# Performance work log

Measured on AMD Instinct MI355X. Metric: run time of the kernel, lower is better.

## Reference

```python
import jax, jax.numpy as jnp
import numpy as np

EPS = 1e-5

def _ln(x, g, b):
    m = jnp.mean(x, axis=-1, keepdims=True)
    v = jnp.var(x, axis=-1, keepdims=True)
    return (x - m) / jnp.sqrt(v + EPS) * g + b

def _lin(x, w, b):
    # torch-style weight [out, in]
    return x @ w.T + b

def _mlp(x, w1, b1, w2, b2):
    # Mlp: Linear -> exact GELU -> Linear (dropout=0)
    return _lin(jax.nn.gelu(_lin(x, w1, b1), approximate=False), w2, b2)

def setup_inputs() -> dict:
    B, C, H, W = 2, 256, 64, 64
    key = jax.random.key(0)
    ks = jax.random.split(key, 32)
    s = 0.02  # param init scale keeps attention logits in a sane range
    d = {
        'center_fea': jax.random.normal(ks[0], (B, C, H, W), jnp.float32),
        'wh_fea':     jax.random.normal(ks[1], (B, C, H, W), jnp.float32),
        'cls_fea':    jax.random.normal(ks[2], (B, C, H, W), jnp.float32),
        'mix_w': jax.random.normal(ks[3], (C, 3 * C), jnp.float32) * s,
        'mix_b': jnp.zeros((C,), jnp.float32),
        'ln_g': jnp.ones((C,), jnp.float32),
        'ln_b': jnp.zeros((C,), jnp.float32),
        'q1_w': jax.random.normal(ks[4], (C, C), jnp.float32) * s,
        'q1_b': jnp.zeros((C,), jnp.float32),
        'q2_w': jax.random.normal(ks[5], (C, C), jnp.float32) * s,
        'q2_b': jnp.zeros((C,), jnp.float32),
        'q3_w': jax.random.normal(ks[6], (C, C), jnp.float32) * s,
        'q3_b': jnp.zeros((C,), jnp.float32),
        'k_w': jax.random.normal(ks[7], (C, C), jnp.float32) * s,
        'k_b': jnp.zeros((C,), jnp.float32),
        'v_w': jax.random.normal(ks[8], (C, C), jnp.float32) * s,
        'v_b': jnp.zeros((C,), jnp.float32),
        'cmlp_w1': jax.random.normal(ks[9], (C, C), jnp.float32) * s,
        'cmlp_b1': jnp.zeros((C,), jnp.float32),
        'cmlp_w2': jax.random.normal(ks[10], (C, C), jnp.float32) * s,
        'cmlp_b2': jnp.zeros((C,), jnp.float32),
        'wmlp_w1': jax.random.normal(ks[11], (C, C), jnp.float32) * s,
        'wmlp_b1': jnp.zeros((C,), jnp.float32),
        'wmlp_w2': jax.random.normal(ks[12], (C, C), jnp.float32) * s,
        'wmlp_b2': jnp.zeros((C,), jnp.float32),
        'clsmlp_w1': jax.random.normal(ks[13], (C, C), jnp.float32) * s,
        'clsmlp_b1': jnp.zeros((C,), jnp.float32),
        'clsmlp_w2': jax.random.normal(ks[14], (C, C), jnp.float32) * s,
        'clsmlp_b2': jnp.zeros((C,), jnp.float32),
    }
    return d

def reference(center_fea, wh_fea, cls_fea, mix_w, mix_b, ln_g, ln_b,
              q1_w, q1_b, q2_w, q2_b, q3_w, q3_b, k_w, k_b, v_w, v_b,
              cmlp_w1, cmlp_b1, cmlp_w2, cmlp_b2,
              wmlp_w1, wmlp_b1, wmlp_w2, wmlp_b2,
              clsmlp_w1, clsmlp_b1, clsmlp_w2, clsmlp_b2):
    b, c, h, w = center_fea.shape
    # 1x1 conv mix over concatenated channels [b, 3c, h, w] -> [b, c, h, w]
    cat = jnp.concatenate([center_fea, wh_fea, cls_fea], axis=1)
    mix = jnp.einsum('oc,bchw->bohw', mix_w, cat) + mix_b[None, :, None, None]

    tok = lambda x: x.reshape(b, c, h * w).transpose(0, 2, 1)  # [b, N, c]
    cf, wf, clf, mf = tok(center_fea), tok(wh_fea), tok(cls_fea), tok(mix)

    ct, wt, clt, mt = _ln(cf, ln_g, ln_b), _ln(wf, ln_g, ln_b), _ln(clf, ln_g, ln_b), _ln(mf, ln_g, ln_b)

    kf = _lin(mt, k_w, k_b)  # shared K
    vf = _lin(mt, v_w, v_b)  # shared V

    def attend(q):
        score = jax.nn.softmax(jnp.einsum('bnd,bmd->bnm', q, kf), axis=-1)  # [b, N, N]
        return jnp.einsum('bnm,bmd->bnd', score, vf)

    cf  = _ln(cf  + attend(_lin(ct,  q1_w, q1_b)), ln_g, ln_b)
    wf  = _ln(wf  + attend(_lin(wt,  q2_w, q2_b)), ln_g, ln_b)
    clf = _ln(clf + attend(_lin(clt, q3_w, q3_b)), ln_g, ln_b)

    cf  = _ln(cf  + _mlp(cf,  cmlp_w1, cmlp_b1, cmlp_w2, cmlp_b2), ln_g, ln_b)
    wf  = _ln(wf  + _mlp(wf,  wmlp_w1, wmlp_b1, wmlp_w2, wmlp_b2), ln_g, ln_b)
    clf = _ln(clf + _mlp(clf, clsmlp_w1, clsmlp_b1, clsmlp_w2, clsmlp_b2), ln_g, ln_b)

    untok = lambda x: x.transpose(0, 2, 1).reshape(b, c, h, w)
    return (untok(cf), untok(wf), untok(clf))
```

## Files before the change

### kernel.cpp

```cpp
#include <hip/hip_runtime.h>
#include <hip/hip_bf16.h>
#include <math.h>

typedef unsigned int   u32;
typedef unsigned short u16;
typedef float floatx4 __attribute__((ext_vector_type(4)));
typedef short bf16x8  __attribute__((ext_vector_type(8)));

#define MFMA16(a,b,c) __builtin_amdgcn_mfma_f32_16x16x32_bf16((a),(b),(c),0,0,0)

static __device__ __forceinline__ float bfbits2f(u16 h){
    return __uint_as_float(((u32)h) << 16);
}
static __device__ __forceinline__ u16 f2bfbits(float f){
    u32 u = __float_as_uint(f);
    u32 r = (u + 0x7fffu + ((u >> 16) & 1u)) >> 16;
    return (u16)r;
}
static __device__ __forceinline__ bool sniff_bf16(const void* ln_g){
    return ((const u32*)ln_g)[0] == 0x3f803f80u;
}

typedef __attribute__((address_space(1))) const unsigned int gas_u32;
typedef __attribute__((address_space(3))) unsigned int las_u32;
static __device__ __forceinline__ void gl_lds16(const void* g, void* l){
    __builtin_amdgcn_global_load_lds((gas_u32*)g, (las_u32*)l, 16, 0, 0);
}

#define DPPF(v, ctrl) __uint_as_float((u32)__builtin_amdgcn_update_dpp( \
        (int)__float_as_uint(v), (int)__float_as_uint(v), (ctrl), 0xf, 0xf, true))

static __device__ __forceinline__ float red16_max(float v){
    v = fmaxf(v, DPPF(v, 0xB1));
    v = fmaxf(v, DPPF(v, 0x4E));
    v = fmaxf(v, DPPF(v, 0x141));
    v = fmaxf(v, DPPF(v, 0x140));
    return v;
}
static __device__ __forceinline__ float red16_sum(float v){
    v += DPPF(v, 0xB1);
    v += DPPF(v, 0x4E);
    v += DPPF(v, 0x141);
    v += DPPF(v, 0x140);
    return v;
}

struct PackJob { const void* src; void* dst; int n; int mode; };
struct PackParams { PackJob jobs[26]; const void* lng; };

__global__ __launch_bounds__(256) void k_pack(PackParams p){
    bool isb = sniff_bf16(p.lng);
    PackJob j = p.jobs[blockIdx.y];
    for (int i = blockIdx.x * 256 + threadIdx.x; i < j.n; i += 256 * 256){
        float v = isb ? bfbits2f(((const u16*)j.src)[i]) : ((const float*)j.src)[i];
        if (j.mode == 0) ((u16*)j.dst)[i]  = f2bfbits(v);
        else             ((float*)j.dst)[i] = v;
    }
}

struct FtParams { const void* src[3]; u16* dst[3]; const void* lng; };

__global__ __launch_bounds__(256) void k_feat_t(FtParams p){
    bool isb = sniff_bf16(p.lng);
    int z = blockIdx.z; int si = z >> 1; int b = z & 1;
    const void* src = p.src[si]; u16* dst = p.dst[si];
    int n0 = blockIdx.x * 64, c0 = blockIdx.y * 64;
    __shared__ float tile[64][65];
    int t = threadIdx.x; int tx = t & 63; int ty = t >> 6;
    #pragma unroll
    for (int pp = 0; pp < 16; ++pp){
        int cl = ty + pp * 4;
        size_t off = ((size_t)b * 256 + c0 + cl) * 4096 + n0 + tx;
        float v = isb ? bfbits2f(((const u16*)src)[off]) : ((const float*)src)[off];
        tile[cl][tx] = v;
    }
    __syncthreads();
    #pragma unroll
    for (int pp = 0; pp < 16; ++pp){
        int nl = ty + pp * 4; int cl = tx;
        dst[((size_t)b * 4096 + n0 + nl) * 256 + c0 + cl] = f2bfbits(tile[cl][nl]);
    }
}

struct GemmJob { const u16* A0; const u16* A1; const u16* A2;
                 const u16* W; const float* bias; const u16* res; u16* out; };
struct GemmParams { GemmJob jobs[5]; int K; int op; };

__global__ __launch_bounds__(256, 4) void k_gemm(GemmParams p){
    GemmJob j = p.jobs[blockIdx.z];
    int m0 = blockIdx.x * 64, n0 = blockIdx.y * 64;
    __shared__ __align__(16) u16 As[2][64][64];
    __shared__ __align__(16) u16 Bs[2][64][64];
    int t = threadIdx.x;
    int wave = t >> 6, lane = t & 63, l15 = lane & 15, quad = lane >> 4;
    int mh = (wave & 1) * 32, nh = (wave >> 1) * 32;
    int key = l15 & 7;

    auto stage = [&](int bi, int k0){
        const u16* Ap = (k0 < 256) ? j.A0 : (k0 < 512 ? j.A1 : j.A2);
        int koff = k0 & 255;
        #pragma unroll
        for (int i = 0; i < 2; ++i){
            int rq = wave * 2 + i;
            int r  = rq * 8 + (lane >> 3);
            int gs = (lane & 7) ^ (r & 7);
            gl_lds16(Ap  + (size_t)(m0 + r) * 256 + koff + gs * 8, &As[bi][rq * 8][0]);
            gl_lds16(j.W + (size_t)(n0 + r) * p.K + k0   + gs * 8, &Bs[bi][rq * 8][0]);
        }
    };

    floatx4 acc[2][2];
    #pragma unroll
    for (int a = 0; a < 2; ++a)
        #pragma unroll
        for (int bq = 0; bq < 2; ++bq) acc[a][bq] = (floatx4){0.f,0.f,0.f,0.f};

    stage(0, 0);
    __syncthreads();
    int nk = p.K >> 6, buf = 0;

    for (int ks = 0; ks < nk; ++ks){
        if (ks + 1 < nk) stage(buf ^ 1, (ks + 1) * 64);
        #pragma unroll
        for (int kc = 0; kc < 2; ++kc){
            int gsel = ((kc * 4 + quad) ^ key) * 8;
            bf16x8 a0 = *(const bf16x8*)&As[buf][mh +      l15][gsel];
            bf16x8 a1 = *(const bf16x8*)&As[buf][mh + 16 + l15][gsel];
            bf16x8 b0 = *(const bf16x8*)&Bs[buf][nh +      l15][gsel];
            bf16x8 b1 = *(const bf16x8*)&Bs[buf][nh + 16 + l15][gsel];
            acc[0][0] = MFMA16(a0, b0, acc[0][0]);
            acc[0][1] = MFMA16(a0, b1, acc[0][1]);
            acc[1][0] = MFMA16(a1, b0, acc[1][0]);
            acc[1][1] = MFMA16(a1, b1, acc[1][1]);
        }
        __syncthreads();
        buf ^= 1;
    }

    #pragma unroll
    for (int mb = 0; mb < 2; ++mb)
        #pragma unroll
        for (int nb = 0; nb < 2; ++nb){
            int col = n0 + nh + nb * 16 + l15;
            float bias = j.bias[col];
            #pragma unroll
            for (int rg = 0; rg < 4; ++rg){
                int row = m0 + mh + mb * 16 + quad * 4 + rg;
                float v = acc[mb][nb][rg] + bias;
                if (p.op == 1)      v = 0.5f * v * (1.0f + erff(v * 0.70710678118f));
                else if (p.op == 2) v += bfbits2f(j.res[(size_t)row * 256 + col]);
                j.out[(size_t)row * 256 + col] = f2bfbits(v);
            }
        }
}

struct LnJob { const u16* src; u16* dst; };
struct LnParams { LnJob jobs[4]; const float* g; const float* b; };

__global__ __launch_bounds__(256, 4) void k_ln(LnParams p){
    LnJob j = p.jobs[blockIdx.y];
    int g16 = threadIdx.x >> 4, l = threadIdx.x & 15;
    size_t tok = (size_t)blockIdx.x * 16 + g16;
    const u16* row = j.src + tok * 256 + l * 16;
    uint4 ra = *(const uint4*)(row);
    uint4 rb = *(const uint4*)(row + 8);
    u32 wv[8] = {ra.x, ra.y, ra.z, ra.w, rb.x, rb.y, rb.z, rb.w};
    float va[16];
    float s1 = 0.f, s2 = 0.f;
    #pragma unroll
    for (int i = 0; i < 8; ++i){
        float a = bfbits2f((u16)(wv[i] & 0xffffu));
        float c = bfbits2f((u16)(wv[i] >> 16));
        va[2*i] = a; va[2*i+1] = c;
        s1 += a + c; s2 += a*a + c*c;
    }
    s1 = red16_sum(s1); s2 = red16_sum(s2);
    float mean = s1 * (1.f/256.f);
    float var  = s2 * (1.f/256.f) - mean * mean;
    float rstd = rsqrtf(var + 1e-5f);
    int c0 = l * 16;
    u32 ow[8];
    #pragma unroll
    for (int i = 0; i < 8; ++i){
        float x0 = (va[2*i]   - mean) * rstd * p.g[c0 + 2*i]     + p.b[c0 + 2*i];
        float x1 = (va[2*i+1] - mean) * rstd * p.g[c0 + 2*i + 1] + p.b[c0 + 2*i + 1];
        ow[i] = (u32)f2bfbits(x0) | ((u32)f2bfbits(x1) << 16);
    }
    u16* dst = j.dst + tok * 256 + c0;
    *(uint4*)(dst)     = (uint4){ow[0], ow[1], ow[2], ow[3]};
    *(uint4*)(dst + 8) = (uint4){ow[4], ow[5], ow[6], ow[7]};
}

struct LnOutParams { const u16* Z[3]; void* out; const float* g; const float* b; const void* lng; };

__global__ __launch_bounds__(256, 4) void k_ln_out(LnOutParams p){
    bool isb = sniff_bf16(p.lng);
    int y = blockIdx.y; int s = y >> 1, b = y & 1;
    const u16* Z = p.Z[s] + (size_t)b * 4096 * 256;
    int tok0 = blockIdx.x * 64;
    __shared__ u16 tile[64][258];
    int t = threadIdx.x, g16 = t >> 4, l = t & 15;
    #pragma unroll
    for (int pass = 0; pass < 4; ++pass){
        int tl = pass * 16 + g16;
        const u16* row = Z + (size_t)(tok0 + tl) * 256 + l * 16;
        uint4 ra = *(const uint4*)(row);
        uint4 rb = *(const uint4*)(row + 8);
        u32 wv[8] = {ra.x, ra.y, ra.z, ra.w, rb.x, rb.y, rb.z, rb.w};
        float va[16];
        float s1 = 0.f, s2 = 0.f;
        #pragma unroll
        for (int i = 0; i < 8; ++i){
            float a = bfbits2f((u16)(wv[i] & 0xffffu));
            float c = bfbits2f((u16)(wv[i] >> 16));
            va[2*i] = a; va[2*i+1] = c;
            s1 += a + c; s2 += a*a + c*c;
        }
        s1 = red16_sum(s1); s2 = red16_sum(s2);
        float mean = s1 * (1.f/256.f);
        float var  = s2 * (1.f/256.f) - mean * mean;
        float rstd = rsqrtf(var + 1e-5f);
        int c0 = l * 16;
        u32* drow = (u32*)&tile[tl][c0];
        #pragma unroll
        for (int i = 0; i < 8; ++i){
            float x0 = (va[2*i]   - mean) * rstd * p.g[c0 + 2*i]     + p.b[c0 + 2*i];
            float x1 = (va[2*i+1] - mean) * rstd * p.g[c0 + 2*i + 1] + p.b[c0 + 2*i + 1];
            drow[i] = (u32)f2bfbits(x0) | ((u32)f2bfbits(x1) << 16);
        }
    }
    __syncthreads();
    size_t obase = ((size_t)s * 2 + b) * 256 * 4096;
    int cq = t >> 6, tl2 = t & 63;
    #pragma unroll
    for (int pp = 0; pp < 64; ++pp){
        int c = pp * 4 + cq;
        u16 raw = tile[tl2][c];
        size_t off = obase + (size_t)c * 4096 + tok0 + tl2;
        if (isb) ((u16*)p.out)[off]   = raw;
        else     ((float*)p.out)[off] = bfbits2f(raw);
    }
}

__global__ __launch_bounds__(256, 4) void k_vt(const u16* __restrict__ Vf, u16* __restrict__ Vt){
    int b = blockIdx.z;
    int n0 = blockIdx.x * 64, c0 = blockIdx.y * 64;
    __shared__ u16 tile[64][66];
    int t = threadIdx.x; int tx = t & 63; int ty = t >> 6;
    #pragma unroll
    for (int pp = 0; pp < 16; ++pp){
        int nl = ty + pp * 4;
        tile[nl][tx] = Vf[((size_t)b * 4096 + n0 + nl) * 256 + c0 + tx];
    }
    __syncthreads();
    #pragma unroll
    for (int pp = 0; pp < 16; ++pp){
        int cl = ty + pp * 4; int nl = tx;
        Vt[((size_t)b * 256 + c0 + cl) * 4096 + n0 + nl] = tile[nl][cl];
    }
}

struct FlashParams {
    const u16* Q[3]; const u16* K; const u16* Vt;
    const u16* Res[3]; u16* Out[3];
    const float* g; const float* b;
};

__global__ __launch_bounds__(256, 2) void k_flash(FlashParams p){
    int s = blockIdx.y >> 1, b = blockIdx.y & 1;
    int m0 = blockIdx.x * 64;
    const u16* Q   = p.Q[s]   + (size_t)b * 4096 * 256;
    const u16* Kf  = p.K      + (size_t)b * 4096 * 256;
    const u16* Vtg = p.Vt     + (size_t)b * 256 * 4096;
    const u16* Res = p.Res[s] + (size_t)b * 4096 * 256;
    u16*       Out = p.Out[s] + (size_t)b * 4096 * 256;

    __shared__ __align__(16) u16 Kb[2][32][256];
    __shared__ __align__(16) u16 Vb[2][256][32];
    __shared__ __align__(16) u16 Pl[4][16][40];

    int t = threadIdx.x, wave = t >> 6, lane = t & 63, l15 = lane & 15, quad = lane >> 4;

    auto stage = [&](int bi, int kv0){
        #pragma unroll
        for (int m = 0; m < 4; ++m){
            int q = wave * 4 + m;
            int r0 = q * 2 + (lane >> 5);
            int gg = (lane & 31) ^ (r0 & 7);
            gl_lds16(Kf + (size_t)(kv0 + r0) * 256 + gg * 8, &Kb[bi][q * 2][0]);
        }
        #pragma unroll
        for (int m = 0; m < 4; ++m){
            int q = wave * 4 + m;
            int d = q * 16 + (lane >> 2);
            int gg = (lane & 3) ^ ((d >> 1) & 3);
            gl_lds16(Vtg + (size_t)d * 4096 + kv0 + gg * 8, &Vb[bi][q * 16][0]);
        }
    };

    stage(0, 0);

    bf16x8 qf[8];
    {
        const u16* qrow = Q + (size_t)(m0 + wave * 16 + l15) * 256 + quad * 8;
        #pragma unroll
        for (int kc = 0; kc < 8; ++kc) qf[kc] = *(const bf16x8*)(qrow + kc * 32);
    }
    floatx4 o[16];
    #pragma unroll
    for (int i = 0; i < 16; ++i) o[i] = (floatx4){0.f,0.f,0.f,0.f};
    float mrow[4] = {-INFINITY,-INFINITY,-INFINITY,-INFINITY};
    float lsum[4] = {0.f,0.f,0.f,0.f};

    __syncthreads();
    int buf = 0;

    for (int ch = 0; ch < 128; ++ch){
        if (ch < 127) stage(buf ^ 1, (ch + 1) * 32);

        floatx4 sa[2];
        #pragma unroll
        for (int sub = 0; sub < 2; ++sub){
            int row = sub * 16 + l15;
            floatx4 a0 = (floatx4){0.f,0.f,0.f,0.f};
            floatx4 a1 = (floatx4){0.f,0.f,0.f,0.f};
            #pragma unroll
            for (int kc = 0; kc < 4; ++kc){
                bf16x8 kb0 = *(const bf16x8*)&Kb[buf][row][((((2*kc  ) * 4 + quad) ^ (row & 7))) * 8];
                bf16x8 kb1 = *(const bf16x8*)&Kb[buf][row][((((2*kc+1) * 4 + quad) ^ (row & 7))) * 8];
                a0 = MFMA16(qf[2*kc  ], kb0, a0);
                a1 = MFMA16(qf[2*kc+1], kb1, a1);
            }
            sa[sub] = a0 + a1;
        }

        float al[4]; int grow = 0;
        #pragma unroll
        for (int rg = 0; rg < 4; ++rg){
            float m1 = red16_max(fmaxf(sa[0][rg], sa[1][rg]));
            grow |= (m1 > mrow[rg]) ? 1 : 0;
            float mn = fmaxf(mrow[rg], m1);
            al[rg] = __expf(mrow[rg] - mn);
            mrow[rg] = mn;
        }
        #pragma unroll
        for (int rg = 0; rg < 4; ++rg){
            float p0 = __expf(sa[0][rg] - mrow[rg]);
            float p1 = __expf(sa[1][rg] - mrow[rg]);
            sa[0][rg] = p0; sa[1][rg] = p1;
            lsum[rg] = lsum[rg] * al[rg] + (p0 + p1);
        }

        #pragma unroll
        for (int sub = 0; sub < 2; ++sub)
            #pragma unroll
            for (int rg = 0; rg < 4; ++rg)
                Pl[wave][quad * 4 + rg][sub * 16 + l15] = f2bfbits(sa[sub][rg]);

        if (__any(grow)){
            #pragma unroll
            for (int dc = 0; dc < 16; ++dc)
                #pragma unroll
                for (int rg = 0; rg < 4; ++rg) o[dc][rg] *= al[rg];
        }

        asm volatile("s_waitcnt lgkmcnt(0)" ::: "memory");
        __builtin_amdgcn_sched_barrier(0);

        bf16x8 pa = *(const bf16x8*)&Pl[wave][l15][quad * 8];
        #pragma unroll
        for (int dc = 0; dc < 16; ++dc){
            int row = dc * 16 + l15;
            bf16x8 vb = *(const bf16x8*)&Vb[buf][row][((quad ^ ((row >> 1) & 3))) * 8];
            o[dc] = MFMA16(pa, vb, o[dc]);
        }

        __syncthreads();
        buf ^= 1;
    }

    float inv[4];
    #pragma unroll
    for (int rg = 0; rg < 4; ++rg) inv[rg] = 1.0f / red16_sum(lsum[rg]);
    float s1[4] = {0.f,0.f,0.f,0.f}, s2[4] = {0.f,0.f,0.f,0.f};
    #pragma unroll
    for (int dc = 0; dc < 16; ++dc)
        #pragma unroll
        for (int rg = 0; rg < 4; ++rg){
            int row = m0 + wave * 16 + quad * 4 + rg;
            float v = o[dc][rg] * inv[rg] + bfbits2f(Res[(size_t)row * 256 + dc * 16 + l15]);
            o[dc][rg] = v;
            s1[rg] += v; s2[rg] += v * v;
        }
    #pragma unroll
    for (int rg = 0; rg < 4; ++rg){
        float mean = red16_sum(s1[rg]) * (1.f/256.f);
        float q2   = red16_sum(s2[rg]);
        float var  = q2 * (1.f/256.f) - mean * mean;
        s1[rg] = mean; s2[rg] = rsqrtf(var + 1e-5f);
    }
    #pragma unroll
    for (int dc = 0; dc < 16; ++dc){
        int c = dc * 16 + l15;
        float gv = p.g[c], bv = p.b[c];
        #pragma unroll
        for (int rg = 0; rg < 4; ++rg){
            int row = m0 + wave * 16 + quad * 4 + rg;
            Out[(size_t)row * 256 + c] = f2bfbits((o[dc][rg] - s1[rg]) * s2[rg] * gv + bv);
        }
    }
}

extern "C" void kernel_launch(void* const* d_in, const int* in_sizes, int n_in,
                              void* d_out, int out_size, void* d_ws, size_t ws_size,
                              hipStream_t stream) {
    (void)in_sizes; (void)n_in; (void)out_size; (void)ws_size;
    const size_t SLOT = (size_t)2 * 4096 * 256;
    u16* ws = (u16*)d_ws;
    auto slot = [&](int i){ return ws + (size_t)i * SLOT; };

    u16 *Tc = slot(0),  *Tw = slot(1),  *Tcl = slot(2),  *Tm = slot(3);
    u16 *Lc = slot(4),  *Lw = slot(5),  *Lcl = slot(6),  *Lm = slot(7);
    u16 *Q1 = slot(8),  *Q2 = slot(9),  *Q3  = slot(10);
    u16 *Kf = slot(11), *Vf = slot(12), *Vt  = slot(13);
    u16 *Yc = slot(14), *Yw = slot(15), *Ycl = slot(16);
    u16 *Hc = Q1, *Hw = Q2, *Hcl = Q3;
    u16 *Zc = Lc, *Zw = Lw, *Zcl = Lcl;

    u16* wbase = slot(17);
    u16 *mixw = wbase;
    u16 *q1w = wbase + 196608, *q2w = q1w + 65536, *q3w = q2w + 65536;
    u16 *kw  = q3w + 65536,    *vw  = kw  + 65536;
    u16 *cw1 = vw  + 65536, *cw2 = cw1 + 65536, *ww1 = cw2 + 65536,
        *ww2 = ww1 + 65536, *clw1 = ww2 + 65536, *clw2 = clw1 + 65536;
    float* pbase = (float*)(wbase + 1048576);
    float *mixb = pbase,        *lng = pbase+256,  *lnb = pbase+512,
          *q1b = pbase+768,  *q2b = pbase+1024, *q3b = pbase+1280,
          *kb  = pbase+1536, *vb  = pbase+1792,
          *cb1 = pbase+2048, *cb2 = pbase+2304, *wb1 = pbase+2560,
          *wb2 = pbase+2816, *clb1= pbase+3072, *clb2= pbase+3328;

    {
        PackParams pp;
        const int widx[12] = {3,7,9,11,13,15,17,19,21,23,25,27};
        u16* wdst[12] = {mixw,q1w,q2w,q3w,kw,vw,cw1,cw2,ww1,ww2,clw1,clw2};
        for (int i = 0; i < 12; ++i)
            pp.jobs[i] = PackJob{ d_in[widx[i]], wdst[i], (i==0?196608:65536), 0 };
        const int pidx[14] = {4,5,6,8,10,12,14,16,18,20,22,24,26,28};
        float* pdst[14] = {mixb,lng,lnb,q1b,q2b,q3b,kb,vb,cb1,cb2,wb1,wb2,clb1,clb2};
        for (int i = 0; i < 14; ++i)
            pp.jobs[12+i] = PackJob{ d_in[pidx[i]], pdst[i], 256, 1 };
        pp.lng = d_in[5];
        hipLaunchKernelGGL(k_pack, dim3(256, 26), dim3(256), 0, stream, pp);
    }
    {
        FtParams fp;
        fp.src[0] = d_in[0]; fp.src[1] = d_in[1]; fp.src[2] = d_in[2];
        fp.dst[0] = Tc; fp.dst[1] = Tw; fp.dst[2] = Tcl;
        fp.lng = d_in[5];
        hipLaunchKernelGGL(k_feat_t, dim3(64, 4, 6), dim3(256), 0, stream, fp);
    }
    {
        GemmParams gp; gp.K = 768; gp.op = 0;
        gp.jobs[0] = GemmJob{ Tc, Tw, Tcl, mixw, mixb, nullptr, Tm };
        hipLaunchKernelGGL(k_gemm, dim3(128, 4, 1), dim3(256), 0, stream, gp);
    }
    {
        LnParams lp; lp.g = lng; lp.b = lnb;
        lp.jobs[0] = LnJob{Tc, Lc}; lp.jobs[1] = LnJob{Tw, Lw};
        lp.jobs[2] = LnJob{Tcl, Lcl}; lp.jobs[3] = LnJob{Tm, Lm};
        hipLaunchKernelGGL(k_ln, dim3(512, 4), dim3(256), 0, stream, lp);
    }
    {
        GemmParams gp; gp.K = 256; gp.op = 0;
        gp.jobs[0] = GemmJob{ Lc,  nullptr, nullptr, q1w, q1b, nullptr, Q1 };
        gp.jobs[1] = GemmJob{ Lw,  nullptr, nullptr, q2w, q2b, nullptr, Q2 };
        gp.jobs[2] = GemmJob{ Lcl, nullptr, nullptr, q3w, q3b, nullptr, Q3 };
        gp.jobs[3] = GemmJob{ Lm,  nullptr, nullptr, kw,  kb,  nullptr, Kf };
        gp.jobs[4] = GemmJob{ Lm,  nullptr, nullptr, vw,  vb,  nullptr, Vf };
        hipLaunchKernelGGL(k_gemm, dim3(128, 4, 5), dim3(256), 0, stream, gp);
    }
    hipLaunchKernelGGL(k_vt, dim3(64, 4, 2), dim3(256), 0, stream, Vf, Vt);
    {
        FlashParams fp;
        fp.Q[0] = Q1; fp.Q[1] = Q2; fp.Q[2] = Q3;
        fp.K = Kf; fp.Vt = Vt;
        fp.Res[0] = Tc; fp.Res[1] = Tw; fp.Res[2] = Tcl;
        fp.Out[0] = Yc; fp.Out[1] = Yw; fp.Out[2] = Ycl;
        fp.g = lng; fp.b = lnb;
        hipLaunchKernelGGL(k_flash, dim3(64, 6), dim3(256), 0, stream, fp);
    }
    {
        GemmParams gp; gp.K = 256; gp.op = 1;
        gp.jobs[0] = GemmJob{ Yc,  nullptr, nullptr, cw1,  cb1,  nullptr, Hc };
        gp.jobs[1] = GemmJob{ Yw,  nullptr, nullptr, ww1,  wb1,  nullptr, Hw };
        gp.jobs[2] = GemmJob{ Ycl, nullptr, nullptr, clw1, clb1, nullptr, Hcl };
        hipLaunchKernelGGL(k_gemm, dim3(128, 4, 3), dim3(256), 0, stream, gp);
    }
    {
        GemmParams gp; gp.K = 256; gp.op = 2;
        gp.jobs[0] = GemmJob{ Hc,  nullptr, nullptr, cw2,  cb2,  Yc,  Zc };
        gp.jobs[1] = GemmJob{ Hw,  nullptr, nullptr, ww2,  wb2,  Yw,  Zw };
        gp.jobs[2] = GemmJob{ Hcl, nullptr, nullptr, clw2, clb2, Ycl, Zcl };
        hipLaunchKernelGGL(k_gemm, dim3(128, 4, 3), dim3(256), 0, stream, gp);
    }
    {
        LnOutParams lo;
        lo.Z[0] = Zc; lo.Z[1] = Zw; lo.Z[2] = Zcl;
        lo.out = d_out; lo.g = lng; lo.b = lnb; lo.lng = d_in[5];
        hipLaunchKernelGGL(k_ln_out, dim3(64, 6), dim3(256), 0, stream, lo);
    }
}
```

Baseline: 419.1 us.

## Warp-specialize flash attention with a loader wave and 48-row blocks across streams

```diff
diff --git a/kernel.cpp b/kernel.cpp
--- a/kernel.cpp
+++ b/kernel.cpp
@@ -267,42 +267,46 @@
 };
 
 __global__ __launch_bounds__(256, 2) void k_flash(FlashParams p){
-    int s = blockIdx.y >> 1, b = blockIdx.y & 1;
-    int m0 = blockIdx.x * 64;
-    const u16* Q   = p.Q[s]   + (size_t)b * 4096 * 256;
-    const u16* Kf  = p.K      + (size_t)b * 4096 * 256;
-    const u16* Vtg = p.Vt     + (size_t)b * 256 * 4096;
-    const u16* Res = p.Res[s] + (size_t)b * 4096 * 256;
-    u16*       Out = p.Out[s] + (size_t)b * 4096 * 256;
+    int bx = blockIdx.x, b = blockIdx.y;
+    int t = threadIdx.x, wave = t >> 6, lane = t & 63, l15 = lane & 15, quad = lane >> 4;
+
+    const u16* Kf  = p.K  + (size_t)b * 4096 * 256;
+    const u16* Vtg = p.Vt + (size_t)b * 256 * 4096;
 
     __shared__ __align__(16) u16 Kb[2][32][256];
     __shared__ __align__(16) u16 Vb[2][256][32];
-    __shared__ __align__(16) u16 Pl[4][16][40];
-
-    int t = threadIdx.x, wave = t >> 6, lane = t & 63, l15 = lane & 15, quad = lane >> 4;
+    __shared__ __align__(16) u16 Pl[3][16][40];
 
     auto stage = [&](int bi, int kv0){
         #pragma unroll
-        for (int m = 0; m < 4; ++m){
-            int q = wave * 4 + m;
-            int r0 = q * 2 + (lane >> 5);
+        for (int m = 0; m < 16; ++m){
+            int r0 = m * 2 + (lane >> 5);
             int gg = (lane & 31) ^ (r0 & 7);
-            gl_lds16(Kf + (size_t)(kv0 + r0) * 256 + gg * 8, &Kb[bi][q * 2][0]);
-        }
-        #pragma unroll
-        for (int m = 0; m < 4; ++m){
-            int q = wave * 4 + m;
-            int d = q * 16 + (lane >> 2);
+            gl_lds16(Kf + (size_t)(kv0 + r0) * 256 + gg * 8, &Kb[bi][m * 2][0]);
+        }
+        #pragma unroll
+        for (int m = 0; m < 16; ++m){
+            int d = m * 16 + (lane >> 2);
             int gg = (lane & 3) ^ ((d >> 1) & 3);
-            gl_lds16(Vtg + (size_t)d * 4096 + kv0 + gg * 8, &Vb[bi][q * 16][0]);
+            gl_lds16(Vtg + (size_t)d * 4096 + kv0 + gg * 8, &Vb[bi][m * 16][0]);
         }
     };
 
-    stage(0, 0);
+    int g = bx * 48 + wave * 16;
+    int s = (wave < 3) ? (g >> 12) : 0;
+    int m0 = g & 4095;
+    const u16* Qg  = (s == 0) ? p.Q[0]   : (s == 1 ? p.Q[1]   : p.Q[2]);
+    const u16* Res = (s == 0) ? p.Res[0] : (s == 1 ? p.Res[1] : p.Res[2]);
+    u16*       Out = (s == 0) ? p.Out[0] : (s == 1 ? p.Out[1] : p.Out[2]);
+    Qg  += (size_t)b * 4096 * 256;
+    Res += (size_t)b * 4096 * 256;
+    Out += (size_t)b * 4096 * 256;
+
+    if (wave == 3) stage(0, 0);
 
     bf16x8 qf[8];
-    {
-        const u16* qrow = Q + (size_t)(m0 + wave * 16 + l15) * 256 + quad * 8;
+    if (wave < 3){
+        const u16* qrow = Qg + (size_t)(m0 + l15) * 256 + quad * 8;
         #pragma unroll
         for (int kc = 0; kc < 8; ++kc) qf[kc] = *(const bf16x8*)(qrow + kc * 32);
     }
@@ -316,97 +320,101 @@
     int buf = 0;
 
     for (int ch = 0; ch < 128; ++ch){
-        if (ch < 127) stage(buf ^ 1, (ch + 1) * 32);
-
-        floatx4 sa[2];
-        #pragma unroll
-        for (int sub = 0; sub < 2; ++sub){
-            int row = sub * 16 + l15;
-            floatx4 a0 = (floatx4){0.f,0.f,0.f,0.f};
-            floatx4 a1 = (floatx4){0.f,0.f,0.f,0.f};
-            #pragma unroll
-            for (int kc = 0; kc < 4; ++kc){
-                bf16x8 kb0 = *(const bf16x8*)&Kb[buf][row][((((2*kc  ) * 4 + quad) ^ (row & 7))) * 8];
-                bf16x8 kb1 = *(const bf16x8*)&Kb[buf][row][((((2*kc+1) * 4 + quad) ^ (row & 7))) * 8];
-                a0 = MFMA16(qf[2*kc  ], kb0, a0);
-                a1 = MFMA16(qf[2*kc+1], kb1, a1);
-            }
-            sa[sub] = a0 + a1;
-        }
-
-        float al[4]; int grow = 0;
-        #pragma unroll
-        for (int rg = 0; rg < 4; ++rg){
-            float m1 = red16_max(fmaxf(sa[0][rg], sa[1][rg]));
-            grow |= (m1 > mrow[rg]) ? 1 : 0;
-            float mn = fmaxf(mrow[rg], m1);
-            al[rg] = __expf(mrow[rg] - mn);
-            mrow[rg] = mn;
-        }
-        #pragma unroll
-        for (int rg = 0; rg < 4; ++rg){
-            float p0 = __expf(sa[0][rg] - mrow[rg]);
-            float p1 = __expf(sa[1][rg] - mrow[rg]);
-            sa[0][rg] = p0; sa[1][rg] = p1;
-            lsum[rg] = lsum[rg] * al[rg] + (p0 + p1);
-        }
-
-        #pragma unroll
-        for (int sub = 0; sub < 2; ++sub)
-            #pragma unroll
-            for (int rg = 0; rg < 4; ++rg)
-                Pl[wave][quad * 4 + rg][sub * 16 + l15] = f2bfbits(sa[sub][rg]);
-
-        if (__any(grow)){
-            #pragma unroll
-            for (int dc = 0; dc < 16; ++dc)
+        if (wave == 3){
+            if (ch < 127) stage(buf ^ 1, (ch + 1) * 32);
+        } else {
+            floatx4 sa[2];
+            #pragma unroll
+            for (int sub = 0; sub < 2; ++sub){
+                int row = sub * 16 + l15;
+                floatx4 a0 = (floatx4){0.f,0.f,0.f,0.f};
+                floatx4 a1 = (floatx4){0.f,0.f,0.f,0.f};
                 #pragma unroll
-                for (int rg = 0; rg < 4; ++rg) o[dc][rg] *= al[rg];
-        }
-
-        asm volatile("s_waitcnt lgkmcnt(0)" ::: "memory");
-        __builtin_amdgcn_sched_barrier(0);
-
-        bf16x8 pa = *(const bf16x8*)&Pl[wave][l15][quad * 8];
-        #pragma unroll
-        for (int dc = 0; dc < 16; ++dc){
-            int row = dc * 16 + l15;
-            bf16x8 vb = *(const bf16x8*)&Vb[buf][row][((quad ^ ((row >> 1) & 3))) * 8];
-            o[dc] = MFMA16(pa, vb, o[dc]);
+                for (int kc = 0; kc < 4; ++kc){
+                    bf16x8 kb0 = *(const bf16x8*)&Kb[buf][row][((((2*kc  ) * 4 + quad) ^ (row & 7))) * 8];
+                    bf16x8 kb1 = *(const bf16x8*)&Kb[buf][row][((((2*kc+1) * 4 + quad) ^ (row & 7))) * 8];
+                    a0 = MFMA16(qf[2*kc  ], kb0, a0);
+                    a1 = MFMA16(qf[2*kc+1], kb1, a1);
+                }
+                sa[sub] = a0 + a1;
+            }
+
+            float al[4]; int grow = 0;
+            #pragma unroll
+            for (int rg = 0; rg < 4; ++rg){
+                float m1 = red16_max(fmaxf(sa[0][rg], sa[1][rg]));
+                grow |= (m1 > mrow[rg]) ? 1 : 0;
+                float mn = fmaxf(mrow[rg], m1);
+                al[rg] = __expf(mrow[rg] - mn);
+                mrow[rg] = mn;
+            }
+            #pragma unroll
+            for (int rg = 0; rg < 4; ++rg){
+                float p0 = __expf(sa[0][rg] - mrow[rg]);
+                float p1 = __expf(sa[1][rg] - mrow[rg]);
+                sa[0][rg] = p0; sa[1][rg] = p1;
+                lsum[rg] = lsum[rg] * al[rg] + (p0 + p1);
+            }
+
+            #pragma unroll
+            for (int sub = 0; sub < 2; ++sub)
+                #pragma unroll
+                for (int rg = 0; rg < 4; ++rg)
+                    Pl[wave][quad * 4 + rg][sub * 16 + l15] = f2bfbits(sa[sub][rg]);
+
+            if (__any(grow)){
+                #pragma unroll
+                for (int dc = 0; dc < 16; ++dc)
+                    #pragma unroll
+                    for (int rg = 0; rg < 4; ++rg) o[dc][rg] *= al[rg];
+            }
+
+            asm volatile("s_waitcnt lgkmcnt(0)" ::: "memory");
+            __builtin_amdgcn_sched_barrier(0);
+
+            bf16x8 pa = *(const bf16x8*)&Pl[wave][l15][quad * 8];
+            #pragma unroll
+            for (int dc = 0; dc < 16; ++dc){
+                int row = dc * 16 + l15;
+                bf16x8 vb = *(const bf16x8*)&Vb[buf][row][((quad ^ ((row >> 1) & 3))) * 8];
+                o[dc] = MFMA16(pa, vb, o[dc]);
+            }
         }
 
         __syncthreads();
         buf ^= 1;
     }
 
-    float inv[4];
-    #pragma unroll
-    for (int rg = 0; rg < 4; ++rg) inv[rg] = 1.0f / red16_sum(lsum[rg]);
-    float s1[4] = {0.f,0.f,0.f,0.f}, s2[4] = {0.f,0.f,0.f,0.f};
-    #pragma unroll
-    for (int dc = 0; dc < 16; ++dc)
+    if (wave < 3){
+        float inv[4];
+        #pragma unroll
+        for (int rg = 0; rg < 4; ++rg) inv[rg] = 1.0f / red16_sum(lsum[rg]);
+        float s1[4] = {0.f,0.f,0.f,0.f}, s2[4] = {0.f,0.f,0.f,0.f};
+        #pragma unroll
+        for (int dc = 0; dc < 16; ++dc)
+            #pragma unroll
+            for (int rg = 0; rg < 4; ++rg){
+                int row = m0 + quad * 4 + rg;
+                float v = o[dc][rg] * inv[rg] + bfbits2f(Res[(size_t)row * 256 + dc * 16 + l15]);
+                o[dc][rg] = v;
+                s1[rg] += v; s2[rg] += v * v;
+            }
         #pragma unroll
         for (int rg = 0; rg < 4; ++rg){
-            int row = m0 + wave * 16 + quad * 4 + rg;
-            float v = o[dc][rg] * inv[rg] + bfbits2f(Res[(size_t)row * 256 + dc * 16 + l15]);
-            o[dc][rg] = v;
-            s1[rg] += v; s2[rg] += v * v;
-        }
-    #pragma unroll
-    for (int rg = 0; rg < 4; ++rg){
-        float mean = red16_sum(s1[rg]) * (1.f/256.f);
-        float q2   = red16_sum(s2[rg]);
-        float var  = q2 * (1.f/256.f) - mean * mean;
-        s1[rg] = mean; s2[rg] = rsqrtf(var + 1e-5f);
-    }
-    #pragma unroll
-    for (int dc = 0; dc < 16; ++dc){
-        int c = dc * 16 + l15;
-        float gv = p.g[c], bv = p.b[c];
-        #pragma unroll
-        for (int rg = 0; rg < 4; ++rg){
-            int row = m0 + wave * 16 + quad * 4 + rg;
-            Out[(size_t)row * 256 + c] = f2bfbits((o[dc][rg] - s1[rg]) * s2[rg] * gv + bv);
+            float mean = red16_sum(s1[rg]) * (1.f/256.f);
+            float q2   = red16_sum(s2[rg]);
+            float var  = q2 * (1.f/256.f) - mean * mean;
+            s1[rg] = mean; s2[rg] = rsqrtf(var + 1e-5f);
+        }
+        #pragma unroll
+        for (int dc = 0; dc < 16; ++dc){
+            int c = dc * 16 + l15;
+            float gv = p.g[c], bv = p.b[c];
+            #pragma unroll
+            for (int rg = 0; rg < 4; ++rg){
+                int row = m0 + quad * 4 + rg;
+                Out[(size_t)row * 256 + c] = f2bfbits((o[dc][rg] - s1[rg]) * s2[rg] * gv + bv);
+            }
         }
     }
 }
@@ -488,7 +496,7 @@
         fp.Res[0] = Tc; fp.Res[1] = Tw; fp.Res[2] = Tcl;
         fp.Out[0] = Yc; fp.Out[1] = Yw; fp.Out[2] = Ycl;
         fp.g = lng; fp.b = lnb;
-        hipLaunchKernelGGL(k_flash, dim3(64, 6), dim3(256), 0, stream, fp);
+        hipLaunchKernelGGL(k_flash, dim3(256, 2), dim3(256), 0, stream, fp);
     }
     {
         GemmParams gp; gp.K = 256; gp.op = 1;
```

After: 391.4 us (median of 2 runs). -6.6%, faster.
